# Kernel tuning notes

Hardware: AMD Instinct MI355X
Metric: run time of the kernel (lower is better)

## Reference

```python
import jax, jax.numpy as jnp
import numpy as np

EMBED_DIM = 1024
NUM_HEADS = 16
HEAD_DIM = EMBED_DIM // NUM_HEADS


def setup_inputs() -> dict:
    key = jax.random.key(0)
    ks = jax.random.split(key, 7)
    B, S, D = 8, 1024, EMBED_DIM
    scale = 1.0 / np.sqrt(D)
    x = jax.random.normal(ks[0], (B, S, D), dtype=jnp.float32)
    Wq = jax.random.normal(ks[1], (D, D), dtype=jnp.float32) * scale
    Wk = jax.random.normal(ks[2], (D, D), dtype=jnp.float32) * scale
    Wv = jax.random.normal(ks[3], (D, D), dtype=jnp.float32) * scale
    bq = jax.random.normal(ks[4], (D,), dtype=jnp.float32) * 0.01
    bk = jax.random.normal(ks[5], (D,), dtype=jnp.float32) * 0.01
    bv = jax.random.normal(ks[6], (D,), dtype=jnp.float32) * 0.01
    return {"x": x, "Wq": Wq, "Wk": Wk, "Wv": Wv, "bq": bq, "bk": bk, "bv": bv}


def reference(x, Wq, Wk, Wv, bq, bk, bv):
    B, S, D = x.shape
    H, Hd = NUM_HEADS, HEAD_DIM
    # torch nn.Linear: y = x @ W.T + b
    q = (x @ Wq.T + bq).reshape(B, S, H, Hd).transpose(0, 2, 1, 3)  # [B,H,S,Hd]
    k = (x @ Wk.T + bk).reshape(B, S, H, Hd).transpose(0, 2, 1, 3)
    v = (x @ Wv.T + bv).reshape(B, S, H, Hd).transpose(0, 2, 1, 3)
    scale = Hd ** -0.5
    scores = jnp.einsum('bhqd,bhkd->bhqk', q, k) * scale  # [B,H,S,S]
    attn = jax.nn.softmax(scores, axis=-1)
    # dropout_rate = 0.0 -> identity; out_proj is never applied in the source forward
    ctx = jnp.einsum('bhqk,bhkd->bhqd', attn, v)  # [B,H,S,Hd]
    return ctx.transpose(0, 2, 1, 3).reshape(B, S, D)
```

## Files before the change

### kernel.cpp

```cpp
#include <hip/hip_runtime.h>
#include <hip/hip_bf16.h>
#include <cstdint>
#include <cstddef>


typedef __attribute__((ext_vector_type(8))) short bf16x8;
typedef __attribute__((ext_vector_type(8))) unsigned short u16x8;
typedef __attribute__((ext_vector_type(4))) float f32x4;
typedef __attribute__((ext_vector_type(16))) float f32x16;

typedef const __attribute__((address_space(1))) void* gptr_t;
typedef __attribute__((address_space(3))) void* lptr_t;

#define LOG2E 1.44269504088896340736f

__device__ __forceinline__ unsigned short f2bf(float f) {
  unsigned int u = __float_as_uint(f);
  u += 0x7fffu + ((u >> 16) & 1u);
  return (unsigned short)(u >> 16);
}

__device__ __forceinline__ unsigned int pack_bf16x2(float lo, float hi) {
  const __hip_bfloat162 h = __float22bfloat162_rn(float2{lo, hi});
  unsigned int u;
  __builtin_memcpy(&u, &h, 4);
  return u;
}

__device__ __forceinline__ float vmax16(const f32x16& v) {
  float a = fmaxf(fmaxf(v[0], v[1]), fmaxf(v[2], v[3]));
  float b = fmaxf(fmaxf(v[4], v[5]), fmaxf(v[6], v[7]));
  float c = fmaxf(fmaxf(v[8], v[9]), fmaxf(v[10], v[11]));
  float d = fmaxf(fmaxf(v[12], v[13]), fmaxf(v[14], v[15]));
  return fmaxf(fmaxf(a, b), fmaxf(c, d));
}

__global__ void cvt_f32_bf16(const float* __restrict__ src,
                             unsigned short* __restrict__ dst, int n4) {
  int i = blockIdx.x * blockDim.x + threadIdx.x;
  if (i >= n4) return;
  float4 v = reinterpret_cast<const float4*>(src)[i];
  ushort4 o;
  o.x = f2bf(v.x); o.y = f2bf(v.y); o.z = f2bf(v.z); o.w = f2bf(v.w);
  reinterpret_cast<ushort4*>(dst)[i] = o;
}

__global__ void cvt_w3(const float* __restrict__ wq, const float* __restrict__ wk,
                       const float* __restrict__ wv, unsigned short* __restrict__ dst) {
  const int b = blockIdx.x;
  const int sel = b >> 10;
  const float* src = (sel == 0) ? wq : (sel == 1) ? wk : wv;
  const int i = (b & 1023) * 256 + threadIdx.x;
  float4 v = reinterpret_cast<const float4*>(src)[i];
  ushort4 o;
  o.x = f2bf(v.x); o.y = f2bf(v.y); o.z = f2bf(v.z); o.w = f2bf(v.w);
  reinterpret_cast<ushort4*>(dst + (size_t)sel * 1048576)[i] = o;
}

__global__ __launch_bounds__(256) void qkv_gemm(
    const unsigned short* __restrict__ Xb, const unsigned short* __restrict__ Wb,
    const float* __restrict__ bq, const float* __restrict__ bk,
    const float* __restrict__ bv,
    unsigned short* __restrict__ Qo, unsigned short* __restrict__ Ko,
    unsigned short* __restrict__ Vo) {
  __shared__ unsigned short As[128 * 32];
  __shared__ unsigned short Bs[128 * 32];

  const int tid = threadIdx.x;
  const int lane = tid & 63;
  const int w = tid >> 6;
  const int wr = w >> 1, wc = w & 1;
  const int bm = blockIdx.x & 63;
  const int bn = blockIdx.x >> 6;

  const f32x4 vzero = {0.f, 0.f, 0.f, 0.f};
  f32x4 acc[4][4];
#pragma unroll
  for (int m = 0; m < 4; ++m)
#pragma unroll
    for (int n = 0; n < 4; ++n) acc[m][n] = vzero;

  const int c0 = w * 2, c1 = w * 2 + 1;
  const int srow0 = c0 * 16 + (lane >> 2);
  const int srow1 = c1 * 16 + (lane >> 2);
  const int scol = (lane & 3) * 8;
  const unsigned short* gA0 = Xb + (size_t)(bm * 128 + srow0) * 1024 + scol;
  const unsigned short* gA1 = Xb + (size_t)(bm * 128 + srow1) * 1024 + scol;
  const unsigned short* gB0 = Wb + (size_t)(bn * 128 + srow0) * 1024 + scol;
  const unsigned short* gB1 = Wb + (size_t)(bn * 128 + srow1) * 1024 + scol;
  char* lA0 = (char*)As + c0 * 1024;
  char* lA1 = (char*)As + c1 * 1024;
  char* lB0 = (char*)Bs + c0 * 1024;
  char* lB1 = (char*)Bs + c1 * 1024;

  const int aoff = (wr * 64 + (lane & 15)) * 64 + (lane >> 4) * 16;
  const int boff = (wc * 64 + (lane & 15)) * 64 + (lane >> 4) * 16;

  for (int kt = 0; kt < 32; ++kt) {
    const int k0 = kt * 32;
    __builtin_amdgcn_global_load_lds((gptr_t)(gA0 + k0), (lptr_t)lA0, 16, 0, 0);
    __builtin_amdgcn_global_load_lds((gptr_t)(gA1 + k0), (lptr_t)lA1, 16, 0, 0);
    __builtin_amdgcn_global_load_lds((gptr_t)(gB0 + k0), (lptr_t)lB0, 16, 0, 0);
    __builtin_amdgcn_global_load_lds((gptr_t)(gB1 + k0), (lptr_t)lB1, 16, 0, 0);
    __syncthreads();

    bf16x8 a[4], b[4];
#pragma unroll
    for (int m = 0; m < 4; ++m)
      a[m] = *reinterpret_cast<const bf16x8*>((const char*)As + aoff + m * 16 * 64);
#pragma unroll
    for (int n = 0; n < 4; ++n)
      b[n] = *reinterpret_cast<const bf16x8*>((const char*)Bs + boff + n * 16 * 64);
#pragma unroll
    for (int m = 0; m < 4; ++m)
#pragma unroll
      for (int n = 0; n < 4; ++n)
        acc[m][n] = __builtin_amdgcn_mfma_f32_16x16x32_bf16(a[m], b[n], acc[m][n], 0, 0, 0);
    __syncthreads();
  }

  const int t = bn >> 3;
  const float* bias = (t == 0) ? bq : (t == 1) ? bk : bv;
  unsigned short* dst = (t == 0) ? Qo : (t == 1) ? Ko : Vo;
  const float sc = (t == 0) ? 0.125f : 1.0f;
#pragma unroll
  for (int n = 0; n < 4; ++n) {
    const int gn = bn * 128 + wc * 64 + n * 16 + (lane & 15);
    const int d = gn & 1023;
    const int h = d >> 6, hd = d & 63;
    const float bias_v = bias[d];
#pragma unroll
    for (int m = 0; m < 4; ++m) {
      const int gm0 = bm * 128 + wr * 64 + m * 16 + ((lane >> 4) << 2);
      const int bb = gm0 >> 10;
      const int s0 = gm0 & 1023;
#pragma unroll
      for (int r = 0; r < 4; ++r) {
        dst[(((size_t)bb * 16 + h) * 1024 + (size_t)(s0 + r)) * 64 + hd] =
            f2bf((acc[m][n][r] + bias_v) * sc);
      }
    }
  }
}

__global__ __launch_bounds__(256) void transpose_v(
    const unsigned short* __restrict__ Vn, unsigned short* __restrict__ Vt) {
  __shared__ __align__(16) unsigned short T[64][72];
  const int tid = threadIdx.x;
  const int head = blockIdx.x & 127;
  const int st = blockIdx.x >> 7;
  const unsigned short* src = Vn + (size_t)head * 65536 + (size_t)st * 64 * 64;
  unsigned short* dst = Vt + (size_t)head * 65536 + (size_t)st * 64;
#pragma unroll
  for (int i = 0; i < 2; ++i) {
    const int idx = tid + i * 256;
    const int r = idx >> 3, ch = idx & 7;
    u16x8 v = *reinterpret_cast<const u16x8*>(src + r * 64 + ch * 8);
#pragma unroll
    for (int j = 0; j < 8; ++j)
      T[ch * 8 + j][r ^ (ch << 3)] = (unsigned short)v[j];
  }
  __syncthreads();
#pragma unroll
  for (int i = 0; i < 2; ++i) {
    const int idx = tid + i * 256;
    const int d = idx >> 3, ch = idx & 7;
    u16x8 v = *reinterpret_cast<const u16x8*>(&T[d][(ch ^ (d >> 3)) << 3]);
    *reinterpret_cast<u16x8*>(dst + (size_t)d * 1024 + ch * 8) = v;
  }
}

__global__ __launch_bounds__(256, 3) void attn32(
    const unsigned short* __restrict__ Q, const unsigned short* __restrict__ K,
    const unsigned short* __restrict__ Vt, float* __restrict__ out) {
  __shared__ __align__(16) char smem[2][16384];
  __shared__ __align__(16) char psm[4][4096];

  const int tid = threadIdx.x;
  const int lane = tid & 63;
  const int ln31 = lane & 31;
  const int g = lane >> 5;
  const int w = tid >> 6;
  const int head = blockIdx.x & 127;
  const int qt = blockIdx.x >> 7;

  const unsigned short* Qh = Q + (size_t)head * 65536;
  const unsigned short* Kh = K + (size_t)head * 65536;
  const unsigned short* Vh = Vt + (size_t)head * 65536;

  const int qrow = qt * 128 + w * 32 + ln31;
  bf16x8 qf[4];
#pragma unroll
  for (int dc = 0; dc < 4; ++dc)
    qf[dc] = *reinterpret_cast<const bf16x8*>(Qh + (size_t)qrow * 64 + dc * 16 + g * 8);

  const int lbA = w * 1024 + lane * 16;
  const int lbB = lbA + 4096;
  const int rA = lbA >> 7, rB = lbB >> 7;
  const int cA = ((((lbA >> 4) & 7) ^ (rA & 7)) << 3);
  const int cB = ((((lbB >> 4) & 7) ^ (rB & 7)) << 3);
  const unsigned short* gK0 = Kh + rA * 64 + cA;
  const unsigned short* gK1 = Kh + rB * 64 + cB;
  const unsigned short* gV0 = Vh + rA * 1024 + cA;
  const unsigned short* gV1 = Vh + rB * 1024 + cB;

  {
    char* b0 = smem[0] + w * 1024;
    __builtin_amdgcn_global_load_lds((gptr_t)gK0, (lptr_t)b0, 16, 0, 0);
    __builtin_amdgcn_global_load_lds((gptr_t)gK1, (lptr_t)(b0 + 4096), 16, 0, 0);
    __builtin_amdgcn_global_load_lds((gptr_t)gV0, (lptr_t)(b0 + 8192), 16, 0, 0);
    __builtin_amdgcn_global_load_lds((gptr_t)gV1, (lptr_t)(b0 + 12288), 16, 0, 0);
  }

  float m_ = -3e38f, l_ = 0.f;
  f32x16 acc0, acc1;
#pragma unroll
  for (int i = 0; i < 16; ++i) { acc0[i] = 0.f; acc1[i] = 0.f; }

  const int swz = (ln31 & 7) << 4;
  const int rowb0 = ln31 * 128;
  int boff[4];
#pragma unroll
  for (int dc = 0; dc < 4; ++dc) boff[dc] = ((((dc << 1) | g) << 4) ^ swz);
  int woff[8];
#pragma unroll
  for (int b = 0; b < 8; ++b) woff[b] = ((b << 4) ^ swz);
  char* Pw0 = psm[w] + ln31 * 128 + 8 * g;
  const char* Pr0 = psm[w] + ln31 * 128;

  for (int kt = 0; kt < 16; ++kt) {
    __syncthreads();
    if (kt < 15) {
      char* nb = smem[(kt + 1) & 1] + w * 1024;
      const int k1 = (kt + 1) * 4096, k2 = (kt + 1) * 64;
      __builtin_amdgcn_global_load_lds((gptr_t)(gK0 + k1), (lptr_t)nb, 16, 0, 0);
      __builtin_amdgcn_global_load_lds((gptr_t)(gK1 + k1), (lptr_t)(nb + 4096), 16, 0, 0);
      __builtin_amdgcn_global_load_lds((gptr_t)(gV0 + k2), (lptr_t)(nb + 8192), 16, 0, 0);
      __builtin_amdgcn_global_load_lds((gptr_t)(gV1 + k2), (lptr_t)(nb + 12288), 16, 0, 0);
    }
    const char* Kb_ = smem[kt & 1] + rowb0;
    const char* Vb_ = Kb_ + 8192;

    f32x16 s0, s1;
#pragma unroll
    for (int i = 0; i < 16; ++i) { s0[i] = 0.f; s1[i] = 0.f; }
    __builtin_amdgcn_s_setprio(1);
#pragma unroll
    for (int dc = 0; dc < 4; ++dc) {
      bf16x8 kf0 = *reinterpret_cast<const bf16x8*>(Kb_ + boff[dc]);
      bf16x8 kf1 = *reinterpret_cast<const bf16x8*>(Kb_ + 4096 + boff[dc]);
      s0 = __builtin_amdgcn_mfma_f32_32x32x16_bf16(kf0, qf[dc], s0, 0, 0, 0);
      s1 = __builtin_amdgcn_mfma_f32_32x32x16_bf16(kf1, qf[dc], s1, 0, 0, 0);
    }
    __builtin_amdgcn_s_setprio(0);

    float tm = fmaxf(vmax16(s0), vmax16(s1));
    tm = fmaxf(tm, __shfl_xor(tm, 32));
    if (__any(tm > m_ + 5.0f)) {
      const float mn = fmaxf(m_, tm);
      const float al = exp2f((m_ - mn) * LOG2E);
      m_ = mn;
      l_ *= al;
#pragma unroll
      for (int i = 0; i < 16; ++i) { acc0[i] *= al; acc1[i] *= al; }
    }
    const float mnl = m_ * LOG2E;
    float ts = 0.f;

#pragma unroll
    for (int b = 0; b < 4; ++b) {
      const float p0 = exp2f(fmaf(s0[4 * b + 0], LOG2E, -mnl));
      const float p1 = exp2f(fmaf(s0[4 * b + 1], LOG2E, -mnl));
      const float p2 = exp2f(fmaf(s0[4 * b + 2], LOG2E, -mnl));
      const float p3 = exp2f(fmaf(s0[4 * b + 3], LOG2E, -mnl));
      ts += (p0 + p1) + (p2 + p3);
      const unsigned long long wp =
          (unsigned long long)pack_bf16x2(p0, p1) |
          ((unsigned long long)pack_bf16x2(p2, p3) << 32);
      *(unsigned long long*)(Pw0 + woff[b]) = wp;
    }
#pragma unroll
    for (int b = 4; b < 8; ++b) {
      const float p0 = exp2f(fmaf(s1[4 * (b - 4) + 0], LOG2E, -mnl));
      const float p1 = exp2f(fmaf(s1[4 * (b - 4) + 1], LOG2E, -mnl));
      const float p2 = exp2f(fmaf(s1[4 * (b - 4) + 2], LOG2E, -mnl));
      const float p3 = exp2f(fmaf(s1[4 * (b - 4) + 3], LOG2E, -mnl));
      ts += (p0 + p1) + (p2 + p3);
      const unsigned long long wp =
          (unsigned long long)pack_bf16x2(p0, p1) |
          ((unsigned long long)pack_bf16x2(p2, p3) << 32);
      *(unsigned long long*)(Pw0 + woff[b]) = wp;
    }
    ts += __shfl_xor(ts, 32);
    l_ += ts;

    bf16x8 pfv[4];
#pragma unroll
    for (int t = 0; t < 4; ++t)
      pfv[t] = *reinterpret_cast<const bf16x8*>(Pr0 + boff[t]);

    __builtin_amdgcn_s_setprio(1);
#pragma unroll
    for (int t = 0; t < 4; ++t) {
      bf16x8 vf0 = *reinterpret_cast<const bf16x8*>(Vb_ + boff[t]);
      bf16x8 vf1 = *reinterpret_cast<const bf16x8*>(Vb_ + 4096 + boff[t]);
      acc0 = __builtin_amdgcn_mfma_f32_32x32x16_bf16(vf0, pfv[t], acc0, 0, 0, 0);
      acc1 = __builtin_amdgcn_mfma_f32_32x32x16_bf16(vf1, pfv[t], acc1, 0, 0, 0);
    }
    __builtin_amdgcn_s_setprio(0);
  }

  const float invl = 1.0f / l_;
  const int bb = head >> 4, hh = head & 15;
  float* orow = out + ((size_t)bb * 1024 + qrow) * 1024 + hh * 64;
#pragma unroll
  for (int rq = 0; rq < 4; ++rq) {
    const int d0 = rq * 8 + g * 4;
    float4 v0, v1;
    v0.x = acc0[rq * 4 + 0] * invl; v0.y = acc0[rq * 4 + 1] * invl;
    v0.z = acc0[rq * 4 + 2] * invl; v0.w = acc0[rq * 4 + 3] * invl;
    v1.x = acc1[rq * 4 + 0] * invl; v1.y = acc1[rq * 4 + 1] * invl;
    v1.z = acc1[rq * 4 + 2] * invl; v1.w = acc1[rq * 4 + 3] * invl;
    *reinterpret_cast<float4*>(orow + d0) = v0;
    *reinterpret_cast<float4*>(orow + 32 + d0) = v1;
  }
}

extern "C" void kernel_launch(void* const* d_in, const int* in_sizes, int n_in,
                              void* d_out, int out_size, void* d_ws, size_t ws_size,
                              hipStream_t stream) {
  const float* x  = (const float*)d_in[0];
  const float* Wq = (const float*)d_in[1];
  const float* Wk = (const float*)d_in[2];
  const float* Wv = (const float*)d_in[3];
  const float* bq = (const float*)d_in[4];
  const float* bk = (const float*)d_in[5];
  const float* bv = (const float*)d_in[6];
  float* out = (float*)d_out;

  char* ws = (char*)d_ws;
  unsigned short* Xb = (unsigned short*)(ws);
  unsigned short* Wb = (unsigned short*)(ws + (size_t)16 * 1024 * 1024);
  unsigned short* Qb = (unsigned short*)(ws + (size_t)22 * 1024 * 1024);
  unsigned short* Kb = Qb + (size_t)8 * 1024 * 1024;
  unsigned short* Vb = Kb + (size_t)8 * 1024 * 1024;
  unsigned short* Vt = Xb;

  cvt_f32_bf16<<<8192, 256, 0, stream>>>(x, Xb, 2097152);
  cvt_w3<<<3072, 256, 0, stream>>>(Wq, Wk, Wv, Wb);

  qkv_gemm<<<1536, 256, 0, stream>>>(Xb, Wb, bq, bk, bv, Qb, Kb, Vb);

  transpose_v<<<2048, 256, 0, stream>>>(Vb, Vt);

  attn32<<<1024, 256, 0, stream>>>(Qb, Kb, Vt, out);
}
```

Before: 161.0 us.

## Rearrange softmax probabilities via cross-lane shuffles instead of LDS round-trip

Measured after the change: 173.6 us. 7.8% more time.

```diff
diff --git a/kernel.cpp b/kernel.cpp
--- a/kernel.cpp
+++ b/kernel.cpp
@@ -8,6 +8,7 @@
 typedef __attribute__((ext_vector_type(8))) unsigned short u16x8;
 typedef __attribute__((ext_vector_type(4))) float f32x4;
 typedef __attribute__((ext_vector_type(16))) float f32x16;
+typedef __attribute__((ext_vector_type(4))) unsigned int u32x4;
 
 typedef const __attribute__((address_space(1))) void* gptr_t;
 typedef __attribute__((address_space(3))) void* lptr_t;
@@ -28,11 +29,14 @@
 }
 
 __device__ __forceinline__ float vmax16(const f32x16& v) {
-  float a = fmaxf(fmaxf(v[0], v[1]), fmaxf(v[2], v[3]));
-  float b = fmaxf(fmaxf(v[4], v[5]), fmaxf(v[6], v[7]));
-  float c = fmaxf(fmaxf(v[8], v[9]), fmaxf(v[10], v[11]));
-  float d = fmaxf(fmaxf(v[12], v[13]), fmaxf(v[14], v[15]));
-  return fmaxf(fmaxf(a, b), fmaxf(c, d));
+  float a = fmaxf(fmaxf(v[0], v[1]), v[2]);
+  float b = fmaxf(fmaxf(v[3], v[4]), v[5]);
+  float c = fmaxf(fmaxf(v[6], v[7]), v[8]);
+  float d = fmaxf(fmaxf(v[9], v[10]), v[11]);
+  float e = fmaxf(fmaxf(v[12], v[13]), v[14]);
+  float f = fmaxf(fmaxf(a, b), v[15]);
+  float h = fmaxf(fmaxf(c, d), e);
+  return fmaxf(f, h);
 }
 
 __global__ void cvt_f32_bf16(const float* __restrict__ src,
@@ -170,11 +174,10 @@
   }
 }
 
-__global__ __launch_bounds__(256, 3) void attn32(
+__global__ __launch_bounds__(256, 5) void attn32(
     const unsigned short* __restrict__ Q, const unsigned short* __restrict__ K,
     const unsigned short* __restrict__ Vt, float* __restrict__ out) {
   __shared__ __align__(16) char smem[2][16384];
-  __shared__ __align__(16) char psm[4][4096];
 
   const int tid = threadIdx.x;
   const int lane = tid & 63;
@@ -222,11 +225,6 @@
   int boff[4];
 #pragma unroll
   for (int dc = 0; dc < 4; ++dc) boff[dc] = ((((dc << 1) | g) << 4) ^ swz);
-  int woff[8];
-#pragma unroll
-  for (int b = 0; b < 8; ++b) woff[b] = ((b << 4) ^ swz);
-  char* Pw0 = psm[w] + ln31 * 128 + 8 * g;
-  const char* Pr0 = psm[w] + ln31 * 128;
 
   for (int kt = 0; kt < 16; ++kt) {
     __syncthreads();
@@ -267,6 +265,7 @@
     const float mnl = m_ * LOG2E;
     float ts = 0.f;
 
+    unsigned int c_[8][2];
 #pragma unroll
     for (int b = 0; b < 4; ++b) {
       const float p0 = exp2f(fmaf(s0[4 * b + 0], LOG2E, -mnl));
@@ -274,10 +273,8 @@
       const float p2 = exp2f(fmaf(s0[4 * b + 2], LOG2E, -mnl));
       const float p3 = exp2f(fmaf(s0[4 * b + 3], LOG2E, -mnl));
       ts += (p0 + p1) + (p2 + p3);
-      const unsigned long long wp =
-          (unsigned long long)pack_bf16x2(p0, p1) |
-          ((unsigned long long)pack_bf16x2(p2, p3) << 32);
-      *(unsigned long long*)(Pw0 + woff[b]) = wp;
+      c_[b][0] = pack_bf16x2(p0, p1);
+      c_[b][1] = pack_bf16x2(p2, p3);
     }
 #pragma unroll
     for (int b = 4; b < 8; ++b) {
@@ -286,26 +283,29 @@
       const float p2 = exp2f(fmaf(s1[4 * (b - 4) + 2], LOG2E, -mnl));
       const float p3 = exp2f(fmaf(s1[4 * (b - 4) + 3], LOG2E, -mnl));
       ts += (p0 + p1) + (p2 + p3);
-      const unsigned long long wp =
-          (unsigned long long)pack_bf16x2(p0, p1) |
-          ((unsigned long long)pack_bf16x2(p2, p3) << 32);
-      *(unsigned long long*)(Pw0 + woff[b]) = wp;
+      c_[b][0] = pack_bf16x2(p0, p1);
+      c_[b][1] = pack_bf16x2(p2, p3);
     }
     ts += __shfl_xor(ts, 32);
     l_ += ts;
 
-    bf16x8 pfv[4];
-#pragma unroll
-    for (int t = 0; t < 4; ++t)
-      pfv[t] = *reinterpret_cast<const bf16x8*>(Pr0 + boff[t]);
-
     __builtin_amdgcn_s_setprio(1);
 #pragma unroll
     for (int t = 0; t < 4; ++t) {
+      u32x4 pv;
+#pragma unroll
+      for (int i = 0; i < 2; ++i) {
+        const unsigned int A = c_[2 * t][i], Bv = c_[2 * t + 1][i];
+        const unsigned int y =
+            (unsigned int)__shfl_xor((int)((g == 0) ? Bv : A), 32);
+        pv[i]     = (g == 0) ? A : y;
+        pv[i + 2] = (g == 0) ? y : Bv;
+      }
+      const bf16x8 pfv = __builtin_bit_cast(bf16x8, pv);
       bf16x8 vf0 = *reinterpret_cast<const bf16x8*>(Vb_ + boff[t]);
       bf16x8 vf1 = *reinterpret_cast<const bf16x8*>(Vb_ + 4096 + boff[t]);
-      acc0 = __builtin_amdgcn_mfma_f32_32x32x16_bf16(vf0, pfv[t], acc0, 0, 0, 0);
-      acc1 = __builtin_amdgcn_mfma_f32_32x32x16_bf16(vf1, pfv[t], acc1, 0, 0, 0);
+      acc0 = __builtin_amdgcn_mfma_f32_32x32x16_bf16(vf0, pfv, acc0, 0, 0, 0);
+      acc1 = __builtin_amdgcn_mfma_f32_32x32x16_bf16(vf1, pfv, acc1, 0, 0, 0);
     }
     __builtin_amdgcn_s_setprio(0);
   }
```
